# Kernel tuning notes

Hardware: AMD Instinct MI355X
Metric: run time of the kernel (lower is better)

The kernel has to match this reference:

```python
import jax, jax.numpy as jnp
import numpy as np

SEQ_LEN = 2048
N_FFT = 4096  # nearest power of two >= 2*SEQ_LEN - 1
K = 24
D_IN = 512
D_OUT = 512
K_U = 3


def setup_inputs() -> dict:
    key = jax.random.key(0)
    k1, k2, k3, k4, k5 = jax.random.split(key, 5)
    x = jax.random.normal(k1, (1, SEQ_LEN, D_IN), dtype=jnp.float32)
    phi = jax.random.normal(k2, (SEQ_LEN, K), dtype=jnp.float32)
    M = jax.random.normal(k3, (D_OUT, D_IN, K_U), dtype=jnp.float32) / D_IN
    M_phi_plus = jax.random.normal(k4, (K, D_IN, D_OUT), dtype=jnp.float32) / 10.0
    M_phi_minus = jax.random.normal(k5, (K, D_IN, D_OUT), dtype=jnp.float32) / 10.0
    return {"x": x, "phi": phi, "M": M, "M_phi_plus": M_phi_plus, "M_phi_minus": M_phi_minus}


def _convolve(u, v, n):
    # u: (bsz, seq, d_in); v: (seq, K) spectral filters
    bsz, seq_len, d_in = u.shape
    Kf = v.shape[1]
    # alternating sign (+1, -1, +1, ...) along time, shape (1, seq, 1, 1)
    sgn = jnp.where(jnp.arange(seq_len) % 2 == 1, -1.0, 1.0).reshape(1, seq_len, 1, 1)
    v_f = jnp.fft.rfft(v.astype(jnp.float32).reshape(1, seq_len, Kf, 1, 1), n=n, axis=1)
    u_exp = jnp.broadcast_to(u[:, :, None, :], (bsz, seq_len, Kf, d_in))
    # stack [u, u*sgn] -> (bsz, seq, K, d_in, 2)
    U = jnp.stack([u_exp, u_exp * sgn], axis=-1).astype(jnp.float32)
    U_f = jnp.fft.rfft(U, n=n, axis=1)
    U_conv = jnp.fft.irfft(v_f * U_f, n=n, axis=1)[:, :seq_len]
    U_plus = U_conv[..., 0]
    U_minus = U_conv[..., 1] * sgn  # (b, seq, K, d_in) * (1, seq, 1, 1)
    return U_plus, U_minus


def _ar_preds(M, x):
    # M: (d_out, d_in, k_u); x: (b, l, d_in)
    # ar[t] = sum_{i=0}^{k_u-1} M[:,:,i] @ x[t-i]  (zero before start)
    b, l, _ = x.shape
    out = jnp.zeros((b, l, M.shape[0]), dtype=x.dtype)
    for i in range(M.shape[-1]):
        x_shift = jnp.pad(x, ((0, 0), (i, 0), (0, 0)))[:, :l]
        out = out + jnp.einsum("bli,oi->blo", x_shift, M[:, :, i])
    return out


def reference(x, phi, M, M_phi_plus, M_phi_minus):
    U_plus, U_minus = _convolve(x, phi, N_FFT)
    spectral_plus = jnp.einsum("blkd,kdo->blo", U_plus, M_phi_plus)
    spectral_minus = jnp.einsum("blkd,kdo->blo", U_minus, M_phi_minus)
    output = spectral_plus + spectral_minus  # use_hankel_L=False
    ar = _ar_preds(M, x)
    return output + ar
```

## Files before the change

### kernel.cpp

```cpp
#include <hip/hip_runtime.h>

typedef __bf16 bf16;
typedef bf16 bf16x8 __attribute__((ext_vector_type(8)));
typedef float floatx16 __attribute__((ext_vector_type(16)));

#define AS1 __attribute__((address_space(1)))
#define AS3 __attribute__((address_space(3)))

#define NKB 408

__device__ __forceinline__ void stage_tile(const bf16* g, int ld, bf16* lds, int tid) {
#pragma unroll
    for (int it = 0; it < 4; ++it) {
        int q    = it * 256 + tid;
        int row  = q >> 3;
        int col8 = (q & 7) ^ (row & 7);
        __builtin_amdgcn_global_load_lds(
            (const AS1 void*)(g + (size_t)row * ld + col8 * 8),
            (AS3 void*)(lds + q * 8), 16, 0, 0);
    }
}

__device__ __forceinline__ void mfma_block(const bf16* lA, const bf16* lB,
                                           floatx16 acc[2][2], int lane, int wm, int wn) {
    const int lrow = lane & 31;
    const int lk   = lane >> 5;
#pragma unroll
    for (int s = 0; s < 4; ++s) {
        bf16x8 af[2], bfr[2];
        const int c8 = s * 2 + lk;
#pragma unroll
        for (int mi = 0; mi < 2; ++mi) {
            int r = wm * 64 + mi * 32 + lrow;
            af[mi] = *(const bf16x8*)(lA + r * 64 + ((c8 ^ (r & 7)) << 3));
        }
#pragma unroll
        for (int ni = 0; ni < 2; ++ni) {
            int r = wn * 64 + ni * 32 + lrow;
            bfr[ni] = *(const bf16x8*)(lB + r * 64 + ((c8 ^ (r & 7)) << 3));
        }
#pragma unroll
        for (int mi = 0; mi < 2; ++mi)
#pragma unroll
            for (int ni = 0; ni < 2; ++ni)
                acc[mi][ni] = __builtin_amdgcn_mfma_f32_32x32x16_bf16(
                    af[mi], bfr[ni], acc[mi][ni], 0, 0, 0);
    }
}

#define CD_ROW(r, lane) (((r) & 3) + 8 * ((r) >> 2) + 4 * ((lane) >> 5))

__global__ __launch_bounds__(256) void conv_gemm(const bf16* __restrict__ Tb,
                                                 const bf16* __restrict__ xT2,
                                                 bf16* __restrict__ A2) {
    __shared__ bf16 lA[128 * 64], lB[128 * 64];
    const int tid = threadIdx.x;
    const int lane = tid & 63, wave = tid >> 6, wm = wave & 1, wn = wave >> 1;
    const int bid = blockIdx.x;
    const int a    = 7 - (bid / 384);
    const int rem  = bid % 384;
    const int dblk = rem / 48;
    const int kw   = rem % 48;

    floatx16 acc[2][2];
#pragma unroll
    for (int mi = 0; mi < 2; ++mi)
#pragma unroll
        for (int ni = 0; ni < 2; ++ni)
#pragma unroll
            for (int e = 0; e < 16; ++e) acc[mi][ni][e] = 0.f;

    for (int c = 0; c <= a; ++c) {
        const bf16* Ab = Tb + ((size_t)kw * 8 + (a - c)) * 16384;
        const bf16* Bb = xT2 + (size_t)(dblk * 128) * 1024 + c * 128;
#pragma unroll
        for (int kk = 0; kk < 128; kk += 64) {
            stage_tile(Ab + kk, 128, lA, tid);
            stage_tile(Bb + kk, 1024, lB, tid);
            __syncthreads();
            mfma_block(lA, lB, acc, lane, wm, wn);
            __syncthreads();
        }
    }
    const int w = kw & 1, k = kw >> 1;
    const int kv = w ? (24 + k) : k;
    const int p = dblk >> 2;
    const int kb = kv * 8 + (dblk & 3) * 2 + wn;
#pragma unroll
    for (int mi = 0; mi < 2; ++mi)
#pragma unroll
        for (int ni = 0; ni < 2; ++ni)
#pragma unroll
            for (int r = 0; r < 16; ++r) {
                int tau = a * 128 + wm * 64 + mi * 32 + CD_ROW(r, lane);
                int t = 2 * tau + p + w;
                if (t < 2048) {
                    A2[((size_t)(t >> 7) * NKB + kb) * 8192 + (t & 127) * 64
                       + ni * 32 + (lane & 31)] = (bf16)acc[mi][ni][r];
                }
            }
}

__global__ __launch_bounds__(256) void proj_gemm(const bf16* __restrict__ A2,
                                                 const bf16* __restrict__ B2,
                                                 float* __restrict__ P2) {
    __shared__ bf16 lA[2][128 * 64], lB[2][128 * 64];
    const int tid = threadIdx.x;
    const int lane = tid & 63, wave = tid >> 6, wm = wave & 1, wn = wave >> 1;
    const int bm = blockIdx.x, sp = blockIdx.y, bn = blockIdx.z;
    const bf16* Abase = A2 + ((size_t)bm * NKB + sp * 51) * 8192;
    const bf16* Bbase = B2 + ((size_t)bn * NKB + sp * 51) * 8192;

    floatx16 acc[2][2];
#pragma unroll
    for (int mi = 0; mi < 2; ++mi)
#pragma unroll
        for (int ni = 0; ni < 2; ++ni)
#pragma unroll
            for (int e = 0; e < 16; ++e) acc[mi][ni][e] = 0.f;

    stage_tile(Abase, 64, lA[0], tid);
    stage_tile(Bbase, 64, lB[0], tid);
    __syncthreads();
    int cur = 0;
    for (int ti = 0; ti < 51; ++ti) {
        if (ti + 1 < 51) {
            stage_tile(Abase + (size_t)(ti + 1) * 8192, 64, lA[cur ^ 1], tid);
            stage_tile(Bbase + (size_t)(ti + 1) * 8192, 64, lB[cur ^ 1], tid);
        }
        mfma_block(lA[cur], lB[cur], acc, lane, wm, wn);
        __syncthreads();
        cur ^= 1;
    }
    float* Pt = P2 + (size_t)sp * 1048576;
#pragma unroll
    for (int mi = 0; mi < 2; ++mi)
#pragma unroll
        for (int ni = 0; ni < 2; ++ni)
#pragma unroll
            for (int r = 0; r < 16; ++r) {
                int t = bm * 128 + wm * 64 + mi * 32 + CD_ROW(r, lane);
                int o = bn * 128 + wn * 64 + ni * 32 + (lane & 31);
                Pt[(size_t)t * 512 + o] = acc[mi][ni][r];
            }
}

__global__ void prep_all(const float* __restrict__ x, const float* __restrict__ phi,
                         const float* __restrict__ M, const float* __restrict__ Mp,
                         const float* __restrict__ Mm, bf16* __restrict__ xT2,
                         bf16* __restrict__ A2, bf16* __restrict__ B2,
                         bf16* __restrict__ Tb) {
    __shared__ float smem[2][64 * 65];
    const int b = blockIdx.x, tid = threadIdx.x;
    if (b < 256) {
        int dpt = (b >> 4) * 64, st = (b & 15) * 64;
        int p = dpt >> 9, dbase = dpt & 511;
#pragma unroll
        for (int it = 0; it < 16; ++it) {
            int q = it * 256 + tid;
            int r = q >> 6, cc = q & 63;
            smem[0][r * 65 + cc] = x[(size_t)(2 * (st + r) + p) * 512 + dbase + cc];
        }
        __syncthreads();
#pragma unroll
        for (int it = 0; it < 2; ++it) {
            int q = it * 256 + tid;
            int r = q >> 3, c8 = q & 7;
            bf16x8 v;
#pragma unroll
            for (int jj = 0; jj < 8; ++jj)
                v[jj] = (bf16)smem[0][(c8 * 8 + jj) * 65 + r];
            *(bf16x8*)&xT2[(size_t)(dpt + r) * 1024 + st + c8 * 8] = v;
        }
    } else if (b < 1792) {
        int idx8 = (b - 256) * 256 + tid;
        int t = idx8 / 192, q = idx8 % 192;
        int i = q >> 6, d8 = (q & 63) * 8;
        bf16x8 v;
        if (t - i >= 0) {
            const float* xp = x + (size_t)(t - i) * 512 + d8;
            float4 f0 = *(const float4*)(xp);
            float4 f1 = *(const float4*)(xp + 4);
            v[0] = (bf16)f0.x; v[1] = (bf16)f0.y; v[2] = (bf16)f0.z; v[3] = (bf16)f0.w;
            v[4] = (bf16)f1.x; v[5] = (bf16)f1.y; v[6] = (bf16)f1.z; v[7] = (bf16)f1.w;
        } else {
#pragma unroll
            for (int jj = 0; jj < 8; ++jj) v[jj] = (bf16)0.f;
        }
        int kb = 384 + i * 8 + (d8 >> 6);
        *(bf16x8*)(A2 + ((size_t)(t >> 7) * NKB + kb) * 8192
                      + (t & 127) * 64 + (d8 & 63)) = v;
    } else if (b < 3328) {
        int b2 = b - 1792;
        int k = b2 >> 6, rem2 = b2 & 63;
        int dt = (rem2 >> 3) * 64, ot = (rem2 & 7) * 64;
        const float* Sp = Mp + (size_t)k * 262144;
        const float* Sm = Mm + (size_t)k * 262144;
#pragma unroll
        for (int it = 0; it < 16; ++it) {
            int q = it * 256 + tid;
            int r = q >> 6, cc = q & 63;
            smem[0][r * 65 + cc] = Sp[(size_t)(dt + r) * 512 + ot + cc];
            smem[1][r * 65 + cc] = Sm[(size_t)(dt + r) * 512 + ot + cc];
        }
        __syncthreads();
        int kb = k * 8 + (rem2 >> 3);
#pragma unroll
        for (int it = 0; it < 2; ++it) {
            int q = it * 256 + tid;
            int r = q >> 3, c8 = q & 7;
            bf16x8 vs, vd;
#pragma unroll
            for (int jj = 0; jj < 8; ++jj) {
                float av = smem[0][(c8 * 8 + jj) * 65 + r];
                float bv = smem[1][(c8 * 8 + jj) * 65 + r];
                vs[jj] = (bf16)(av + bv);
                vd[jj] = (bf16)(av - bv);
            }
            int o = ot + r;
            size_t rowoff = (size_t)(o & 127) * 64 + c8 * 8;
            size_t base = (size_t)(o >> 7) * NKB;
            *(bf16x8*)&B2[(base + kb) * 8192 + rowoff]       = vs;
            *(bf16x8*)&B2[(base + kb + 192) * 8192 + rowoff] = vd;
        }
    } else if (b < 3840) {
        int o = b - 3328;
        for (int q = tid; q < 1536; q += 256) smem[0][q] = M[(size_t)o * 1536 + q];
        __syncthreads();
        if (tid < 192) {
            int q = tid * 8;
            int i = q >> 9, d0 = q & 511;
            bf16x8 v;
#pragma unroll
            for (int jj = 0; jj < 8; ++jj) v[jj] = (bf16)smem[0][(d0 + jj) * 3 + i];
            *(bf16x8*)&B2[((size_t)(o >> 7) * NKB + 384 + (tid >> 3)) * 8192
                          + (o & 127) * 64 + (tid & 7) * 8] = v;
        }
    } else if (b < 4224) {
        int b3 = b - 3840;
        int kw = b3 >> 3, m = b3 & 7;
        int k = kw >> 1, w = kw & 1;
        if (tid < 255) {
            int sh = m * 128 - 127 + tid;
            smem[0][tid] = (sh >= 0) ? phi[(size_t)(2 * sh + w) * 24 + k] : 0.f;
        }
        __syncthreads();
        bf16* Tp = Tb + (size_t)b3 * 16384;
#pragma unroll
        for (int it = 0; it < 8; ++it) {
            int q = it * 256 + tid;
            int i = q >> 4, j8 = (q & 15) * 8;
            bf16x8 v;
#pragma unroll
            for (int jj = 0; jj < 8; ++jj)
                v[jj] = (bf16)smem[0][127 + i - (j8 + jj)];
            *(bf16x8*)(Tp + i * 128 + j8) = v;
        }
    } else {
        int idx = (b - 4224) * 2048 + tid * 8;
        int kb = 192 + (idx >> 6), colk = idx & 63;
        bf16x8 z;
#pragma unroll
        for (int jj = 0; jj < 8; ++jj) z[jj] = (bf16)0.f;
        *(bf16x8*)(A2 + (size_t)kb * 8192 + colk) = z;
    }
}

__global__ void reduce8(const float* __restrict__ P2, float* __restrict__ out) {
    int idx = blockIdx.x * 256 + threadIdx.x;
    if (idx >= 2048 * 512) return;
    float s = 0.f;
#pragma unroll
    for (int sp = 0; sp < 8; ++sp)
        s += P2[(size_t)sp * 1048576 + idx];
    out[idx] = s;
}

extern "C" void kernel_launch(void* const* d_in, const int* in_sizes, int n_in,
                              void* d_out, int out_size, void* d_ws, size_t ws_size,
                              hipStream_t stream) {
    const float* x   = (const float*)d_in[0];
    const float* phi = (const float*)d_in[1];
    const float* M   = (const float*)d_in[2];
    const float* Mp  = (const float*)d_in[3];
    const float* Mm  = (const float*)d_in[4];
    float* out = (float*)d_out;
    char* ws = (char*)d_ws;

    bf16*  Tb  = (bf16*)(ws + 0);
    bf16*  xT2 = (bf16*)(ws + 12582912);
    bf16*  A2  = (bf16*)(ws + 14680064);
    bf16*  B2  = (bf16*)(ws + 121634816);
    float* P2  = (float*)(ws + 148373504);

    prep_all<<<4230, 256, 0, stream>>>(x, phi, M, Mp, Mm, xT2, A2, B2, Tb);
    conv_gemm<<<3072, 256, 0, stream>>>(Tb, xT2, A2);
    proj_gemm<<<dim3(16, 8, 4), 256, 0, stream>>>(A2, B2, P2);
    reduce8<<<4096, 256, 0, stream>>>(P2, out);
}
```

Baseline: 262.0 us.

## Share Toeplitz tile across both parities in conv GEMM; atomic split-K reduction

The conv GEMM now processes both even/odd time parities (two B tiles) per block, so each Toeplitz A tile is loaded once and used for twice the MFMA work, halving the block count. The split-K projection writes partials with atomicAdd directly into a zeroed output, which removes the P2 workspace round-trip and the separate reduce kernel. The output is zeroed by extra blocks in prep_all. The cost is more registers and LDS per conv block, atomic contention on the output, and a nondeterministic summation order.

```diff
diff --git a/kernel.cpp b/kernel.cpp
--- a/kernel.cpp
+++ b/kernel.cpp
@@ -48,62 +48,99 @@
     }
 }
 
+__device__ __forceinline__ void mfma_block2(const bf16* lA, const bf16* lB0,
+                                            const bf16* lB1, floatx16 acc[2][2][2],
+                                            int lane, int wm, int wn) {
+    const int lrow = lane & 31;
+    const int lk   = lane >> 5;
+#pragma unroll
+    for (int s = 0; s < 4; ++s) {
+        bf16x8 af[2], b0[2], b1[2];
+        const int c8 = s * 2 + lk;
+#pragma unroll
+        for (int mi = 0; mi < 2; ++mi) {
+            int r = wm * 64 + mi * 32 + lrow;
+            af[mi] = *(const bf16x8*)(lA + r * 64 + ((c8 ^ (r & 7)) << 3));
+        }
+#pragma unroll
+        for (int ni = 0; ni < 2; ++ni) {
+            int r = wn * 64 + ni * 32 + lrow;
+            b0[ni] = *(const bf16x8*)(lB0 + r * 64 + ((c8 ^ (r & 7)) << 3));
+            b1[ni] = *(const bf16x8*)(lB1 + r * 64 + ((c8 ^ (r & 7)) << 3));
+        }
+#pragma unroll
+        for (int mi = 0; mi < 2; ++mi)
+#pragma unroll
+            for (int ni = 0; ni < 2; ++ni) {
+                acc[0][mi][ni] = __builtin_amdgcn_mfma_f32_32x32x16_bf16(
+                    af[mi], b0[ni], acc[0][mi][ni], 0, 0, 0);
+                acc[1][mi][ni] = __builtin_amdgcn_mfma_f32_32x32x16_bf16(
+                    af[mi], b1[ni], acc[1][mi][ni], 0, 0, 0);
+            }
+    }
+}
+
 #define CD_ROW(r, lane) (((r) & 3) + 8 * ((r) >> 2) + 4 * ((lane) >> 5))
 
-__global__ __launch_bounds__(256) void conv_gemm(const bf16* __restrict__ Tb,
-                                                 const bf16* __restrict__ xT2,
-                                                 bf16* __restrict__ A2) {
-    __shared__ bf16 lA[128 * 64], lB[128 * 64];
+__global__ __launch_bounds__(256, 3) void conv_gemm(const bf16* __restrict__ Tb,
+                                                    const bf16* __restrict__ xT2,
+                                                    bf16* __restrict__ A2) {
+    __shared__ bf16 lA[128 * 64], lB[2][128 * 64];
     const int tid = threadIdx.x;
     const int lane = tid & 63, wave = tid >> 6, wm = wave & 1, wn = wave >> 1;
     const int bid = blockIdx.x;
-    const int a    = 7 - (bid / 384);
-    const int rem  = bid % 384;
-    const int dblk = rem / 48;
-    const int kw   = rem % 48;
-
-    floatx16 acc[2][2];
-#pragma unroll
-    for (int mi = 0; mi < 2; ++mi)
-#pragma unroll
-        for (int ni = 0; ni < 2; ++ni)
-#pragma unroll
-            for (int e = 0; e < 16; ++e) acc[mi][ni][e] = 0.f;
+    const int a     = 7 - (bid / 192);
+    const int rem   = bid % 192;
+    const int dhalf = rem / 48;
+    const int kw    = rem % 48;
+
+    floatx16 acc[2][2][2];
+#pragma unroll
+    for (int pp = 0; pp < 2; ++pp)
+#pragma unroll
+        for (int mi = 0; mi < 2; ++mi)
+#pragma unroll
+            for (int ni = 0; ni < 2; ++ni)
+#pragma unroll
+                for (int e = 0; e < 16; ++e) acc[pp][mi][ni][e] = 0.f;
 
     for (int c = 0; c <= a; ++c) {
-        const bf16* Ab = Tb + ((size_t)kw * 8 + (a - c)) * 16384;
-        const bf16* Bb = xT2 + (size_t)(dblk * 128) * 1024 + c * 128;
+        const bf16* Ab  = Tb + ((size_t)kw * 8 + (a - c)) * 16384;
+        const bf16* Bb0 = xT2 + (size_t)(dhalf * 128) * 1024 + c * 128;
+        const bf16* Bb1 = xT2 + (size_t)((dhalf + 4) * 128) * 1024 + c * 128;
 #pragma unroll
         for (int kk = 0; kk < 128; kk += 64) {
             stage_tile(Ab + kk, 128, lA, tid);
-            stage_tile(Bb + kk, 1024, lB, tid);
+            stage_tile(Bb0 + kk, 1024, lB[0], tid);
+            stage_tile(Bb1 + kk, 1024, lB[1], tid);
             __syncthreads();
-            mfma_block(lA, lB, acc, lane, wm, wn);
+            mfma_block2(lA, lB[0], lB[1], acc, lane, wm, wn);
             __syncthreads();
         }
     }
     const int w = kw & 1, k = kw >> 1;
     const int kv = w ? (24 + k) : k;
-    const int p = dblk >> 2;
-    const int kb = kv * 8 + (dblk & 3) * 2 + wn;
-#pragma unroll
-    for (int mi = 0; mi < 2; ++mi)
-#pragma unroll
-        for (int ni = 0; ni < 2; ++ni)
-#pragma unroll
-            for (int r = 0; r < 16; ++r) {
-                int tau = a * 128 + wm * 64 + mi * 32 + CD_ROW(r, lane);
-                int t = 2 * tau + p + w;
-                if (t < 2048) {
-                    A2[((size_t)(t >> 7) * NKB + kb) * 8192 + (t & 127) * 64
-                       + ni * 32 + (lane & 31)] = (bf16)acc[mi][ni][r];
+    const int kb = kv * 8 + dhalf * 2 + wn;
+#pragma unroll
+    for (int pp = 0; pp < 2; ++pp)
+#pragma unroll
+        for (int mi = 0; mi < 2; ++mi)
+#pragma unroll
+            for (int ni = 0; ni < 2; ++ni)
+#pragma unroll
+                for (int r = 0; r < 16; ++r) {
+                    int tau = a * 128 + wm * 64 + mi * 32 + CD_ROW(r, lane);
+                    int t = 2 * tau + pp + w;
+                    if (t < 2048) {
+                        A2[((size_t)(t >> 7) * NKB + kb) * 8192 + (t & 127) * 64
+                           + ni * 32 + (lane & 31)] = (bf16)acc[pp][mi][ni][r];
+                    }
                 }
-            }
 }
 
 __global__ __launch_bounds__(256) void proj_gemm(const bf16* __restrict__ A2,
                                                  const bf16* __restrict__ B2,
-                                                 float* __restrict__ P2) {
+                                                 float* __restrict__ out) {
     __shared__ bf16 lA[2][128 * 64], lB[2][128 * 64];
     const int tid = threadIdx.x;
     const int lane = tid & 63, wave = tid >> 6, wm = wave & 1, wn = wave >> 1;
@@ -132,7 +169,6 @@
         __syncthreads();
         cur ^= 1;
     }
-    float* Pt = P2 + (size_t)sp * 1048576;
 #pragma unroll
     for (int mi = 0; mi < 2; ++mi)
 #pragma unroll
@@ -141,7 +177,7 @@
             for (int r = 0; r < 16; ++r) {
                 int t = bm * 128 + wm * 64 + mi * 32 + CD_ROW(r, lane);
                 int o = bn * 128 + wn * 64 + ni * 32 + (lane & 31);
-                Pt[(size_t)t * 512 + o] = acc[mi][ni][r];
+                atomicAdd(out + (size_t)t * 512 + o, acc[mi][ni][r]);
             }
 }
 
@@ -149,7 +185,7 @@
                          const float* __restrict__ M, const float* __restrict__ Mp,
                          const float* __restrict__ Mm, bf16* __restrict__ xT2,
                          bf16* __restrict__ A2, bf16* __restrict__ B2,
-                         bf16* __restrict__ Tb) {
+                         bf16* __restrict__ Tb, float* __restrict__ out) {
     __shared__ float smem[2][64 * 65];
     const int b = blockIdx.x, tid = threadIdx.x;
     if (b < 256) {
@@ -256,24 +292,19 @@
                 v[jj] = (bf16)smem[0][127 + i - (j8 + jj)];
             *(bf16x8*)(Tp + i * 128 + j8) = v;
         }
-    } else {
+    } else if (b < 4230) {
         int idx = (b - 4224) * 2048 + tid * 8;
         int kb = 192 + (idx >> 6), colk = idx & 63;
         bf16x8 z;
 #pragma unroll
         for (int jj = 0; jj < 8; ++jj) z[jj] = (bf16)0.f;
         *(bf16x8*)(A2 + (size_t)kb * 8192 + colk) = z;
-    }
-}
-
-__global__ void reduce8(const float* __restrict__ P2, float* __restrict__ out) {
-    int idx = blockIdx.x * 256 + threadIdx.x;
-    if (idx >= 2048 * 512) return;
-    float s = 0.f;
-#pragma unroll
-    for (int sp = 0; sp < 8; ++sp)
-        s += P2[(size_t)sp * 1048576 + idx];
-    out[idx] = s;
+    } else {
+        int idx = ((b - 4230) * 256 + tid) * 8;
+        float4 z4 = make_float4(0.f, 0.f, 0.f, 0.f);
+        *(float4*)(out + idx)     = z4;
+        *(float4*)(out + idx + 4) = z4;
+    }
 }
 
 extern "C" void kernel_launch(void* const* d_in, const int* in_sizes, int n_in,
@@ -291,10 +322,8 @@
     bf16*  xT2 = (bf16*)(ws + 12582912);
     bf16*  A2  = (bf16*)(ws + 14680064);
     bf16*  B2  = (bf16*)(ws + 121634816);
-    float* P2  = (float*)(ws + 148373504);
-
-    prep_all<<<4230, 256, 0, stream>>>(x, phi, M, Mp, Mm, xT2, A2, B2, Tb);
-    conv_gemm<<<3072, 256, 0, stream>>>(Tb, xT2, A2);
-    proj_gemm<<<dim3(16, 8, 4), 256, 0, stream>>>(A2, B2, P2);
-    reduce8<<<4096, 256, 0, stream>>>(P2, out);
-}
+
+    prep_all<<<4742, 256, 0, stream>>>(x, phi, M, Mp, Mm, xT2, A2, B2, Tb, out);
+    conv_gemm<<<1536, 256, 0, stream>>>(Tb, xT2, A2);
+    proj_gemm<<<dim3(16, 8, 4), 256, 0, stream>>>(A2, B2, out);
+}
```

After: 404.3 us. 54.3% more time.
